# Kernel optimization log

Hardware: AMD Instinct MI355X
Metric: run time of the kernel (lower is better)

The kernel has to match this reference:

```python
import jax, jax.numpy as jnp
import numpy as np

N = 100000
E = 3200000


def gcn_conv(x, src, dst, W, b):
    """PyG GCNConv: symmetric-normalized aggregation with self-loops.
    src/dst already include self-loop edges. Messages flow src -> dst.
    """
    h = x @ W  # [N, F_out]
    # degree over destination index (includes self-loops), per gcn_norm
    deg = jax.ops.segment_sum(jnp.ones_like(dst, dtype=h.dtype), dst, num_segments=N)
    dinv = jnp.where(deg > 0, jax.lax.rsqrt(deg), 0.0)
    norm = dinv[src] * dinv[dst]  # [E+N]
    msg = h[src] * norm[:, None]  # gather + scale
    out = jax.ops.segment_sum(msg, dst, num_segments=N)  # scatter-add
    return out + b


def setup_inputs() -> dict:
    key = jax.random.key(0)
    k1, k2, k3, k4, k5, k6 = jax.random.split(key, 6)
    x = jax.random.normal(k1, (N, 3), dtype=jnp.float32)
    edge_index = jax.random.randint(k2, (2, E), 0, N, dtype=jnp.int64)
    # Glorot-style init for GCN weights, zero bias (PyG defaults)
    W1 = jax.random.normal(k3, (3, 16), dtype=jnp.float32) * (1.0 / np.sqrt(3))
    b1 = jnp.zeros((16,), dtype=jnp.float32)
    W2 = jax.random.normal(k4, (16, 1), dtype=jnp.float32) * (1.0 / np.sqrt(16))
    b2 = jnp.zeros((1,), dtype=jnp.float32)
    return {"x": x, "edge_index": edge_index, "W1": W1, "b1": b1, "W2": W2, "b2": b2}


def reference(x, edge_index, W1, b1, W2, b2):
    # add self-loops once (both layers use the same augmented graph)
    loops = jnp.arange(N, dtype=edge_index.dtype)
    src = jnp.concatenate([edge_index[0], loops])
    dst = jnp.concatenate([edge_index[1], loops])
    h = gcn_conv(x, src, dst, W1, b1)
    h = jax.nn.relu(h)
    h = gcn_conv(h, src, dst, W2, b2)
    return jax.nn.sigmoid(h)
```

## Files before the change

kernel.cpp:

```cpp
#include <hip/hip_runtime.h>
#include <math.h>


#define NPB 256
#define SHIFT 8
#define NB_MAX 512
#define SPLIT 8
#define T1 512
#define EPT 16

#define FSCALE 1024.0f
#define FBIAS  8192
#define FMASK  0x1FFFFFu

static __device__ __forceinline__ long long load_idx(const void* edges, long long pos, int is64) {
    if (is64) return ((const long long*)edges)[pos];
    return (long long)((const int*)edges)[pos];
}

static __device__ __forceinline__ unsigned long long pack3(float x, float y, float z) {
    unsigned long long e0 = (unsigned)(__float2int_rn(x * FSCALE) + FBIAS);
    unsigned long long e1 = (unsigned)(__float2int_rn(y * FSCALE) + FBIAS);
    unsigned long long e2 = (unsigned)(__float2int_rn(z * FSCALE) + FBIAS);
    return e0 | (e1 << 21) | (e2 << 42);
}

__global__ void k_zero_cursor(int* cursor, int nb, const int* e32, int* flag) {
    int i = blockIdx.x * blockDim.x + threadIdx.x;
    if (i < nb) cursor[i] = 0;
    if (i == 0) {
        int is64 = 1;
        for (int k = 0; k < 16; ++k)
            if (e32[2 * k + 1] != 0) { is64 = 0; break; }
        *flag = is64;
    }
}

__global__ void k_bin(const void* edges, const int* __restrict__ flag,
                      int* __restrict__ cursor, unsigned int* __restrict__ bin,
                      long long E, int nb, int cap) {
    __shared__ int hist[NB_MAX];
    __shared__ int base[NB_MAX];
    const int tid = threadIdx.x;
    for (int b = tid; b < nb; b += T1) hist[b] = 0;
    __syncthreads();

    const int is64 = *flag;
    const long long start = (long long)blockIdx.x * ((long long)T1 * EPT);
    unsigned es[EPT], ed[EPT];

    if (is64) {
        const long long* e64 = (const long long*)edges;
#pragma unroll
        for (int j = 0; j < EPT; ++j) {
            long long e = start + j * T1 + tid;
            if (e < E) { es[j] = (unsigned)e64[e]; ed[j] = (unsigned)e64[E + e]; }
            else ed[j] = 0xFFFFFFFFu;
        }
    } else {
        const int* e32 = (const int*)edges;
#pragma unroll
        for (int j = 0; j < EPT; ++j) {
            long long e = start + j * T1 + tid;
            if (e < E) { es[j] = (unsigned)e32[e]; ed[j] = (unsigned)e32[E + e]; }
            else ed[j] = 0xFFFFFFFFu;
        }
    }

#pragma unroll
    for (int j = 0; j < EPT; ++j)
        if (ed[j] != 0xFFFFFFFFu) atomicAdd(&hist[ed[j] >> SHIFT], 1);
    __syncthreads();

    for (int b = tid; b < nb; b += T1) {
        int h = hist[b];
        base[b] = h ? atomicAdd(&cursor[b], h) : 0;
        hist[b] = 0;
    }
    __syncthreads();

#pragma unroll
    for (int j = 0; j < EPT; ++j) {
        if (ed[j] == 0xFFFFFFFFu) continue;
        int bk = (int)(ed[j] >> SHIFT);
        int off = base[bk] + atomicAdd(&hist[bk], 1);
        if (off < cap)
            bin[(long long)bk * cap + off] = ((ed[j] & (NPB - 1)) << 17) | es[j];
    }
}

static __device__ __forceinline__ void sub_range(int cnt, int sub, int* lo, int* hi) {
    int l = (int)(((long long)cnt * sub / SPLIT) & ~3LL);
    int h = (sub == SPLIT - 1) ? cnt : (int)(((long long)cnt * (sub + 1) / SPLIT) & ~3LL);
    *lo = l; *hi = h;
}

__global__ void k_degP(const unsigned int* __restrict__ bin, const int* __restrict__ cursor,
                       int* __restrict__ part, int cap) {
    __shared__ int dcnt[NPB];
    const int tid = threadIdx.x;
    dcnt[tid] = 0;
    __syncthreads();
    const int bk = blockIdx.x >> 3;
    const int sub = blockIdx.x & (SPLIT - 1);
    const int cnt = min(cursor[bk], cap);
    int lo, hi; sub_range(cnt, sub, &lo, &hi);
    const unsigned int* bp = bin + (long long)bk * cap;
    const int len = hi - lo, nvec = len >> 2;
    const uint4* bp4 = (const uint4*)(bp + lo);
    for (int v = tid; v < nvec; v += NPB) {
        uint4 q = bp4[v];
        atomicAdd(&dcnt[q.x >> 17], 1);
        atomicAdd(&dcnt[q.y >> 17], 1);
        atomicAdd(&dcnt[q.z >> 17], 1);
        atomicAdd(&dcnt[q.w >> 17], 1);
    }
    for (int k = lo + (nvec << 2) + tid; k < hi; k += NPB)
        atomicAdd(&dcnt[bp[k] >> 17], 1);
    __syncthreads();
    part[(long long)blockIdx.x * NPB + tid] = dcnt[tid];
}

__global__ void k_degC(const int* __restrict__ part, const float* __restrict__ x,
                       float* __restrict__ dinv, float4* __restrict__ xs, int n) {
    const int tid = threadIdx.x;
    const int bk = blockIdx.x;
    const int i = bk * NPB + tid;
    if (i >= n) return;
    int degE = 0;
#pragma unroll
    for (int s = 0; s < SPLIT; ++s)
        degE += part[(long long)(bk * SPLIT + s) * NPB + tid];
    float di = rsqrtf((float)degE + 1.0f);
    dinv[i] = di;
    xs[i] = make_float4(x[3 * i] * di, x[3 * i + 1] * di, x[3 * i + 2] * di, (float)degE);
}

__global__ void k_agg1P(const unsigned int* __restrict__ bin, const int* __restrict__ cursor,
                        const float4* __restrict__ xs, unsigned long long* __restrict__ part,
                        int cap) {
    __shared__ unsigned long long acc[NPB];
    const int tid = threadIdx.x;
    acc[tid] = 0ull;
    __syncthreads();
    const int bk = blockIdx.x >> 3;
    const int sub = blockIdx.x & (SPLIT - 1);
    const int cnt = min(cursor[bk], cap);
    int lo, hi; sub_range(cnt, sub, &lo, &hi);
    const unsigned int* bp = bin + (long long)bk * cap;
    const int len = hi - lo, nvec = len >> 2;
    const uint4* bp4 = (const uint4*)(bp + lo);
    for (int v = tid; v < nvec; v += NPB) {
        uint4 q = bp4[v];
        float4 v0 = xs[q.x & 0x1FFFFu];
        float4 v1 = xs[q.y & 0x1FFFFu];
        float4 v2 = xs[q.z & 0x1FFFFu];
        float4 v3 = xs[q.w & 0x1FFFFu];
        atomicAdd(&acc[q.x >> 17], pack3(v0.x, v0.y, v0.z));
        atomicAdd(&acc[q.y >> 17], pack3(v1.x, v1.y, v1.z));
        atomicAdd(&acc[q.z >> 17], pack3(v2.x, v2.y, v2.z));
        atomicAdd(&acc[q.w >> 17], pack3(v3.x, v3.y, v3.z));
    }
    for (int k = lo + (nvec << 2) + tid; k < hi; k += NPB) {
        unsigned p = bp[k];
        float4 v = xs[p & 0x1FFFFu];
        atomicAdd(&acc[p >> 17], pack3(v.x, v.y, v.z));
    }
    __syncthreads();
    part[(long long)blockIdx.x * NPB + tid] = acc[tid];
}

__global__ void k_agg1C(const unsigned long long* __restrict__ part,
                        const float* __restrict__ dinv, const float4* __restrict__ xs,
                        const float* __restrict__ W1, const float* __restrict__ b1,
                        const float* __restrict__ W2, float* __restrict__ gs, int n) {
    const int tid = threadIdx.x;
    const int bk = blockIdx.x;
    const int i = bk * NPB + tid;
    if (i >= n) return;
    int f0 = 0, f1 = 0, f2 = 0;
#pragma unroll
    for (int s = 0; s < SPLIT; ++s) {
        unsigned long long p = part[(long long)(bk * SPLIT + s) * NPB + tid];
        f0 += (int)(p & FMASK);
        f1 += (int)((p >> 21) & FMASK);
        f2 += (int)((p >> 42) & FMASK);
    }
    float4 self = xs[i];
    int degE = (int)self.w;
    const float inv = 1.0f / FSCALE;
    float a0 = (float)(f0 - FBIAS * degE) * inv + self.x;
    float a1 = (float)(f1 - FBIAS * degE) * inv + self.y;
    float a2 = (float)(f2 - FBIAS * degE) * inv + self.z;
    float di = dinv[i];
    a0 *= di; a1 *= di; a2 *= di;
    float g = 0.0f;
#pragma unroll
    for (int c = 0; c < 16; ++c) {
        float h = fmaf(a0, W1[c], fmaf(a1, W1[16 + c], fmaf(a2, W1[32 + c], b1[c])));
        h = fmaxf(h, 0.0f);
        g = fmaf(h, W2[c], g);
    }
    gs[i] = g * di;
}

__global__ void k_agg2P(const unsigned int* __restrict__ bin, const int* __restrict__ cursor,
                        const float* __restrict__ gs, float* __restrict__ part, int cap) {
    __shared__ float acc[NPB];
    const int tid = threadIdx.x;
    acc[tid] = 0.0f;
    __syncthreads();
    const int bk = blockIdx.x >> 3;
    const int sub = blockIdx.x & (SPLIT - 1);
    const int cnt = min(cursor[bk], cap);
    int lo, hi; sub_range(cnt, sub, &lo, &hi);
    const unsigned int* bp = bin + (long long)bk * cap;
    const int len = hi - lo, nvec = len >> 2;
    const uint4* bp4 = (const uint4*)(bp + lo);
    for (int v = tid; v < nvec; v += NPB) {
        uint4 q = bp4[v];
        float g0 = gs[q.x & 0x1FFFFu];
        float g1 = gs[q.y & 0x1FFFFu];
        float g2 = gs[q.z & 0x1FFFFu];
        float g3 = gs[q.w & 0x1FFFFu];
        atomicAdd(&acc[q.x >> 17], g0);
        atomicAdd(&acc[q.y >> 17], g1);
        atomicAdd(&acc[q.z >> 17], g2);
        atomicAdd(&acc[q.w >> 17], g3);
    }
    for (int k = lo + (nvec << 2) + tid; k < hi; k += NPB) {
        unsigned p = bp[k];
        atomicAdd(&acc[p >> 17], gs[p & 0x1FFFFu]);
    }
    __syncthreads();
    part[(long long)blockIdx.x * NPB + tid] = acc[tid];
}

__global__ void k_agg2C(const float* __restrict__ part, const float* __restrict__ dinv,
                        const float* __restrict__ gs, const float* __restrict__ b2,
                        float* __restrict__ out, int n) {
    const int tid = threadIdx.x;
    const int bk = blockIdx.x;
    const int i = bk * NPB + tid;
    if (i >= n) return;
    float acc = gs[i];
#pragma unroll
    for (int s = 0; s < SPLIT; ++s)
        acc += part[(long long)(bk * SPLIT + s) * NPB + tid];
    float z = dinv[i] * acc + b2[0];
    out[i] = 1.0f / (1.0f + expf(-z));
}

__global__ void k_detect(const int* e32, int* flag) {
    if (blockIdx.x == 0 && threadIdx.x == 0) {
        int is64 = 1;
        for (int k = 0; k < 16; ++k)
            if (e32[2 * k + 1] != 0) { is64 = 0; break; }
        *flag = is64;
    }
}
__global__ void f_init_deg(float* deg, int n) {
    int i = blockIdx.x * blockDim.x + threadIdx.x;
    if (i < n) deg[i] = 1.0f;
}
__global__ void f_deg(const void* edges, const int* flag, float* deg, long long E) {
    int is64 = *flag;
    long long e = (long long)blockIdx.x * blockDim.x + threadIdx.x;
    if (e < E) atomicAdd(&deg[load_idx(edges, E + e, is64)], 1.0f);
}
__global__ void f_dinv_xs(const float* x, const float* deg, float* dinv, float4* xs,
                          float4* agg3, int n) {
    int i = blockIdx.x * blockDim.x + threadIdx.x;
    if (i < n) {
        float di = rsqrtf(deg[i]);
        dinv[i] = di;
        float4 v = make_float4(x[3 * i] * di, x[3 * i + 1] * di, x[3 * i + 2] * di, 0.0f);
        xs[i] = v; agg3[i] = v;
    }
}
__global__ void f_edge1(const void* edges, const int* flag, const float4* xs,
                        float* agg3, long long E) {
    int is64 = *flag;
    long long e = (long long)blockIdx.x * blockDim.x + threadIdx.x;
    if (e < E) {
        long long s = load_idx(edges, e, is64);
        long long d = load_idx(edges, E + e, is64);
        float4 v = xs[s];
        atomicAdd(&agg3[4 * d + 0], v.x);
        atomicAdd(&agg3[4 * d + 1], v.y);
        atomicAdd(&agg3[4 * d + 2], v.z);
    }
}
__global__ void f_node1(const float* dinv, const float4* agg3, const float* W1,
                        const float* b1, const float* W2, float* gs, float* agg1, int n) {
    int i = blockIdx.x * blockDim.x + threadIdx.x;
    if (i < n) {
        float di = dinv[i];
        float4 a = agg3[i];
        float a0 = a.x * di, a1 = a.y * di, a2 = a.z * di;
        float g = 0.0f;
#pragma unroll
        for (int k = 0; k < 16; ++k) {
            float h = fmaf(a0, W1[k], fmaf(a1, W1[16 + k], fmaf(a2, W1[32 + k], b1[k])));
            h = fmaxf(h, 0.0f);
            g = fmaf(h, W2[k], g);
        }
        float v = g * di;
        gs[i] = v; agg1[i] = v;
    }
}
__global__ void f_edge2(const void* edges, const int* flag, const float* gs,
                        float* agg1, long long E) {
    int is64 = *flag;
    long long e = (long long)blockIdx.x * blockDim.x + threadIdx.x;
    if (e < E) atomicAdd(&agg1[load_idx(edges, E + e, is64)], gs[load_idx(edges, e, is64)]);
}
__global__ void f_final(const float* dinv, const float* agg1, const float* b2,
                        float* out, int n) {
    int i = blockIdx.x * blockDim.x + threadIdx.x;
    if (i < n) {
        float z = dinv[i] * agg1[i] + b2[0];
        out[i] = 1.0f / (1.0f + expf(-z));
    }
}

extern "C" void kernel_launch(void* const* d_in, const int* in_sizes, int n_in,
                              void* d_out, int out_size, void* d_ws, size_t ws_size,
                              hipStream_t stream) {
    const float* x  = (const float*)d_in[0];
    const void*  ei = d_in[1];
    const float* W1 = (const float*)d_in[2];
    const float* b1 = (const float*)d_in[3];
    const float* W2 = (const float*)d_in[4];
    const float* b2 = (const float*)d_in[5];
    float* out = (float*)d_out;

    const long long n = in_sizes[0] / 3;
    const long long E = in_sizes[1] / 2;

    const int T = 256;
    const int gN = (int)((n + T - 1) / T);
    const int gE = (int)((E + T - 1) / T);

    const int nb = (int)((n + NPB - 1) / NPB);
    long long capll = (E / nb) + (E / nb) / 8 + 256;
    const int cap = (int)((capll + 63) / 64 * 64);
    size_t need = n * sizeof(float4)
                + (size_t)nb * SPLIT * NPB * sizeof(float4)
                + (size_t)nb * cap * sizeof(int)
                + 2 * n * sizeof(float)
                + nb * sizeof(int) + 128;

    if (nb <= NB_MAX && n <= (1 << 17) && ws_size >= need) {
        char* p = (char*)d_ws;
        float4* xs   = (float4*)p;       p += n * sizeof(float4);
        char*  partb = p;                p += (size_t)nb * SPLIT * NPB * sizeof(float4);
        unsigned int* bin = (unsigned int*)p; p += (size_t)nb * cap * sizeof(int);
        float* dinv  = (float*)p;        p += n * sizeof(float);
        float* gs    = (float*)p;        p += n * sizeof(float);
        int*   cursor = (int*)p;         p += nb * sizeof(int);
        int*   flag  = (int*)p;

        const long long per_blk = (long long)T1 * EPT;
        const int gB = (int)((E + per_blk - 1) / per_blk);

        k_zero_cursor<<<(nb + T - 1) / T, T, 0, stream>>>(cursor, nb, (const int*)ei, flag);
        k_bin<<<gB, T1, 0, stream>>>(ei, flag, cursor, bin, E, nb, cap);
        k_degP<<<nb * SPLIT, NPB, 0, stream>>>(bin, cursor, (int*)partb, cap);
        k_degC<<<nb, NPB, 0, stream>>>((const int*)partb, x, dinv, xs, (int)n);
        k_agg1P<<<nb * SPLIT, NPB, 0, stream>>>(bin, cursor, xs, (unsigned long long*)partb, cap);
        k_agg1C<<<nb, NPB, 0, stream>>>((const unsigned long long*)partb, dinv, xs, W1, b1, W2, gs, (int)n);
        k_agg2P<<<nb * SPLIT, NPB, 0, stream>>>(bin, cursor, gs, (float*)partb, cap);
        k_agg2C<<<nb, NPB, 0, stream>>>((const float*)partb, dinv, gs, b2, out, (int)n);
    } else {
        char* p = (char*)d_ws;
        float*  deg  = (float*)p;  p += n * sizeof(float);
        float*  dinv = (float*)p;  p += n * sizeof(float);
        float4* xs   = (float4*)p; p += n * sizeof(float4);
        float4* agg3 = (float4*)p; p += n * sizeof(float4);
        float*  gs   = (float*)p;  p += n * sizeof(float);
        float*  agg1 = (float*)p;  p += n * sizeof(float);
        int*    flag = (int*)p;

        k_detect<<<1, 64, 0, stream>>>((const int*)ei, flag);
        f_init_deg<<<gN, T, 0, stream>>>(deg, (int)n);
        f_deg<<<gE, T, 0, stream>>>(ei, flag, deg, E);
        f_dinv_xs<<<gN, T, 0, stream>>>(x, deg, dinv, xs, agg3, (int)n);
        f_edge1<<<gE, T, 0, stream>>>(ei, flag, xs, (float*)agg3, E);
        f_node1<<<gN, T, 0, stream>>>(dinv, agg3, W1, b1, W2, gs, agg1, (int)n);
        f_edge2<<<gE, T, 0, stream>>>(ei, flag, gs, agg1, E);
        f_final<<<gN, T, 0, stream>>>(dinv, agg1, b2, out, (int)n);
    }
}
```

Measured before the change: 156.4 us.

## Fold degree counting into binning kernel via global atomics, drop degP pass

The degree count moves into the binning kernel: each edge does a global atomicAdd on a per-node counter, which removes the separate k_degP pass that re-read the whole bin array. The binning kernel also keeps each edge's rank from the first shared histogram atomic, so the second round of shared atomics and the histogram reset go away. The cost is 3.2M scattered global atomics on a 100K-entry array during binning, plus zeroing that array in the init kernel.

```diff
diff --git a/kernel.cpp b/kernel.cpp
--- a/kernel.cpp
+++ b/kernel.cpp
@@ -25,9 +25,11 @@
     return e0 | (e1 << 21) | (e2 << 42);
 }
 
-__global__ void k_zero_cursor(int* cursor, int nb, const int* e32, int* flag) {
+__global__ void k_zero(int* cursor, int nb, unsigned int* deg, int n,
+                       const int* e32, int* flag) {
     int i = blockIdx.x * blockDim.x + threadIdx.x;
     if (i < nb) cursor[i] = 0;
+    if (i < n) deg[i] = 0u;
     if (i == 0) {
         int is64 = 1;
         for (int k = 0; k < 16; ++k)
@@ -38,6 +40,7 @@
 
 __global__ void k_bin(const void* edges, const int* __restrict__ flag,
                       int* __restrict__ cursor, unsigned int* __restrict__ bin,
+                      unsigned int* __restrict__ deg,
                       long long E, int nb, int cap) {
     __shared__ int hist[NB_MAX];
     __shared__ int base[NB_MAX];
@@ -48,6 +51,7 @@
     const int is64 = *flag;
     const long long start = (long long)blockIdx.x * ((long long)T1 * EPT);
     unsigned es[EPT], ed[EPT];
+    int rank[EPT];
 
     if (is64) {
         const long long* e64 = (const long long*)edges;
@@ -68,14 +72,17 @@
     }
 
 #pragma unroll
-    for (int j = 0; j < EPT; ++j)
-        if (ed[j] != 0xFFFFFFFFu) atomicAdd(&hist[ed[j] >> SHIFT], 1);
+    for (int j = 0; j < EPT; ++j) {
+        if (ed[j] != 0xFFFFFFFFu) {
+            rank[j] = atomicAdd(&hist[ed[j] >> SHIFT], 1);
+            atomicAdd(&deg[ed[j]], 1u);
+        }
+    }
     __syncthreads();
 
     for (int b = tid; b < nb; b += T1) {
         int h = hist[b];
         base[b] = h ? atomicAdd(&cursor[b], h) : 0;
-        hist[b] = 0;
     }
     __syncthreads();
 
@@ -83,7 +90,7 @@
     for (int j = 0; j < EPT; ++j) {
         if (ed[j] == 0xFFFFFFFFu) continue;
         int bk = (int)(ed[j] >> SHIFT);
-        int off = base[bk] + atomicAdd(&hist[bk], 1);
+        int off = base[bk] + rank[j];
         if (off < cap)
             bin[(long long)bk * cap + off] = ((ed[j] & (NPB - 1)) << 17) | es[j];
     }
@@ -95,42 +102,11 @@
     *lo = l; *hi = h;
 }
 
-__global__ void k_degP(const unsigned int* __restrict__ bin, const int* __restrict__ cursor,
-                       int* __restrict__ part, int cap) {
-    __shared__ int dcnt[NPB];
-    const int tid = threadIdx.x;
-    dcnt[tid] = 0;
-    __syncthreads();
-    const int bk = blockIdx.x >> 3;
-    const int sub = blockIdx.x & (SPLIT - 1);
-    const int cnt = min(cursor[bk], cap);
-    int lo, hi; sub_range(cnt, sub, &lo, &hi);
-    const unsigned int* bp = bin + (long long)bk * cap;
-    const int len = hi - lo, nvec = len >> 2;
-    const uint4* bp4 = (const uint4*)(bp + lo);
-    for (int v = tid; v < nvec; v += NPB) {
-        uint4 q = bp4[v];
-        atomicAdd(&dcnt[q.x >> 17], 1);
-        atomicAdd(&dcnt[q.y >> 17], 1);
-        atomicAdd(&dcnt[q.z >> 17], 1);
-        atomicAdd(&dcnt[q.w >> 17], 1);
-    }
-    for (int k = lo + (nvec << 2) + tid; k < hi; k += NPB)
-        atomicAdd(&dcnt[bp[k] >> 17], 1);
-    __syncthreads();
-    part[(long long)blockIdx.x * NPB + tid] = dcnt[tid];
-}
-
-__global__ void k_degC(const int* __restrict__ part, const float* __restrict__ x,
+__global__ void k_degC(const unsigned int* __restrict__ deg, const float* __restrict__ x,
                        float* __restrict__ dinv, float4* __restrict__ xs, int n) {
-    const int tid = threadIdx.x;
-    const int bk = blockIdx.x;
-    const int i = bk * NPB + tid;
+    const int i = blockIdx.x * NPB + threadIdx.x;
     if (i >= n) return;
-    int degE = 0;
-#pragma unroll
-    for (int s = 0; s < SPLIT; ++s)
-        degE += part[(long long)(bk * SPLIT + s) * NPB + tid];
+    int degE = (int)deg[i];
     float di = rsqrtf((float)degE + 1.0f);
     dinv[i] = di;
     xs[i] = make_float4(x[3 * i] * di, x[3 * i + 1] * di, x[3 * i + 2] * di, (float)degE);
@@ -349,6 +325,7 @@
                 + (size_t)nb * SPLIT * NPB * sizeof(float4)
                 + (size_t)nb * cap * sizeof(int)
                 + 2 * n * sizeof(float)
+                + n * sizeof(int)
                 + nb * sizeof(int) + 128;
 
     if (nb <= NB_MAX && n <= (1 << 17) && ws_size >= need) {
@@ -358,16 +335,16 @@
         unsigned int* bin = (unsigned int*)p; p += (size_t)nb * cap * sizeof(int);
         float* dinv  = (float*)p;        p += n * sizeof(float);
         float* gs    = (float*)p;        p += n * sizeof(float);
+        unsigned int* deg = (unsigned int*)p; p += n * sizeof(int);
         int*   cursor = (int*)p;         p += nb * sizeof(int);
         int*   flag  = (int*)p;
 
         const long long per_blk = (long long)T1 * EPT;
         const int gB = (int)((E + per_blk - 1) / per_blk);
 
-        k_zero_cursor<<<(nb + T - 1) / T, T, 0, stream>>>(cursor, nb, (const int*)ei, flag);
-        k_bin<<<gB, T1, 0, stream>>>(ei, flag, cursor, bin, E, nb, cap);
-        k_degP<<<nb * SPLIT, NPB, 0, stream>>>(bin, cursor, (int*)partb, cap);
-        k_degC<<<nb, NPB, 0, stream>>>((const int*)partb, x, dinv, xs, (int)n);
+        k_zero<<<gN, T, 0, stream>>>(cursor, nb, deg, (int)n, (const int*)ei, flag);
+        k_bin<<<gB, T1, 0, stream>>>(ei, flag, cursor, bin, deg, E, nb, cap);
+        k_degC<<<nb, NPB, 0, stream>>>(deg, x, dinv, xs, (int)n);
         k_agg1P<<<nb * SPLIT, NPB, 0, stream>>>(bin, cursor, xs, (unsigned long long*)partb, cap);
         k_agg1C<<<nb, NPB, 0, stream>>>((const unsigned long long*)partb, dinv, xs, W1, b1, W2, gs, (int)n);
         k_agg2P<<<nb * SPLIT, NPB, 0, stream>>>(bin, cursor, gs, (float*)partb, cap);
```

New measurement: 263.9 us. 1.69x slower.
